# Kernel tuning notes

Hardware: AMD Instinct MI355X
Metric: run time of the kernel (lower is better)

The kernel has to match this reference:

```python
import jax, jax.numpy as jnp
import numpy as np

M, IN, OUT, K = 16384, 1024, 1024, 12


def setup_inputs() -> dict:
    key = jax.random.key(0)
    ks = jax.random.split(key, 7)
    x = jax.random.normal(ks[0], (M, IN), dtype=jnp.float32)
    # grid: per-feature linspace(-2,2) plus noise so the per-row sort is nontrivial
    base = jnp.linspace(-2.0, 2.0, K, dtype=jnp.float32)
    grid = jnp.broadcast_to(base, (IN, K)) + 0.3 * jax.random.normal(ks[1], (IN, K), dtype=jnp.float32)
    coeffs = 0.1 * jax.random.normal(ks[2], (IN, K), dtype=jnp.float32)
    knot_alive = 3.0 * jnp.ones((IN, K), dtype=jnp.float32) + 0.5 * jax.random.normal(ks[3], (IN, K), dtype=jnp.float32)
    proj_w = jax.random.normal(ks[4], (OUT, IN), dtype=jnp.float32) / np.sqrt(IN)
    proj_b = jax.random.normal(ks[5], (OUT,), dtype=jnp.float32) * 0.01
    res_w = jax.random.normal(ks[6], (OUT, IN), dtype=jnp.float32) / np.sqrt(IN)
    return {"x": x, "grid": grid, "coeffs": coeffs, "knot_alive": knot_alive,
            "proj_w": proj_w, "proj_b": proj_b, "res_w": res_w}


def _eval_adaptive_spline(x, grid, coeffs, knot_alive):
    # x: (M, in)  grid/coeffs/knot_alive: (in, K)
    K_ = grid.shape[1]
    sort_idx = jnp.argsort(grid, axis=1)
    sorted_grid = jnp.take_along_axis(grid, sort_idx, axis=1)
    sorted_coeffs = jnp.take_along_axis(coeffs, sort_idx, axis=1)
    sorted_alive = jnp.take_along_axis(knot_alive, sort_idx, axis=1)
    masked_coeffs = sorted_coeffs * jax.nn.sigmoid(sorted_alive)  # (in, K)

    grid_min = sorted_grid[:, 0]   # (in,)
    grid_max = sorted_grid[:, -1]  # (in,)
    x_clamped = jnp.minimum(jnp.maximum(x, grid_min[None, :]), grid_max[None, :])
    grid_range = jnp.maximum(grid_max - grid_min, 1e-6)
    x_norm = (x_clamped - grid_min[None, :]) / grid_range[None, :] * (K_ - 1)  # (M, in)
    idx_l = jnp.clip(x_norm.astype(jnp.int32), 0, K_ - 2)  # trunc == floor (x_norm >= 0)
    frac = x_norm - idx_l.astype(x.dtype)

    feat = jnp.arange(x.shape[1])[None, :]  # (1, in)
    c_left = masked_coeffs[feat, idx_l]      # (M, in)
    c_right = masked_coeffs[feat, idx_l + 1]  # (M, in)
    return c_left + frac * (c_right - c_left)


def reference(x, grid, coeffs, knot_alive, proj_w, proj_b, res_w):
    spline_out = _eval_adaptive_spline(x, grid, coeffs, knot_alive)  # (M, in)
    return spline_out @ proj_w.T + proj_b + x @ res_w.T  # (M, out)
```

## Files before the change

### kernel.cpp

```cpp
#include <hip/hip_runtime.h>
#include <hip/hip_bf16.h>

typedef unsigned short u16;
typedef float f32x4 __attribute__((ext_vector_type(4)));
typedef __bf16 bf16x8 __attribute__((ext_vector_type(8)));
typedef u16 u16x8 __attribute__((ext_vector_type(8)));

#define M_DIM 16384
#define IN_DIM 1024
#define OUT_DIM 1024
#define K_KNOTS 12
#define KCAT 2048


__device__ __forceinline__ u16 f2bf(float f) {
    unsigned int u = __builtin_bit_cast(unsigned int, f);
    u = u + 0x7FFFu + ((u >> 16) & 1u);
    return (u16)(u >> 16);
}

__device__ __forceinline__ void gload_lds16(const void* g, void* l) {
    __builtin_amdgcn_global_load_lds(
        (const __attribute__((address_space(1))) unsigned int*)g,
        (__attribute__((address_space(3))) unsigned int*)l, 16, 0, 0);
}

__global__ __launch_bounds__(256) void prep_conv_kernel(
    const float* __restrict__ grid,
    const float* __restrict__ coeffs,
    const float* __restrict__ alive,
    const float* __restrict__ pw,
    const float* __restrict__ rw,
    float* __restrict__ pmc,
    float* __restrict__ pgmin,
    float* __restrict__ pscale,
    u16* __restrict__ Bw)
{
    const int tid = threadIdx.x;
    if (blockIdx.x < 256) {
        const int n16 = blockIdx.x >> 2;
        const int jb  = (blockIdx.x & 3) * 4;
        #pragma unroll 1
        for (int j = jb; j < jb + 4; ++j) {
            int s = j * 256 + tid;
            int kc = s >> 6, l = s & 63;
            int row = n16 * 16 + (l & 15);
            int k = kc * 32 + ((l >> 4) & 3) * 8;
            const float* src = (k < IN_DIM) ? &pw[(long)row * IN_DIM + k]
                                            : &rw[(long)row * IN_DIM + (k - IN_DIM)];
            float4 v0 = *(const float4*)src;
            float4 v1 = *(const float4*)(src + 4);
            u16x8 ov;
            ov[0] = f2bf(v0.x); ov[1] = f2bf(v0.y); ov[2] = f2bf(v0.z); ov[3] = f2bf(v0.w);
            ov[4] = f2bf(v1.x); ov[5] = f2bf(v1.y); ov[6] = f2bf(v1.z); ov[7] = f2bf(v1.w);
            *(u16x8*)&Bw[((long)n16 * 64 + kc) * 512 + l * 8] = ov;
        }
    } else {
        int i = (blockIdx.x - 256) * 256 + tid;
        if (i >= IN_DIM) return;
        float g[K_KNOTS], c[K_KNOTS], a[K_KNOTS];
        for (int k = 0; k < K_KNOTS; ++k) {
            g[k] = grid[i * K_KNOTS + k];
            c[k] = coeffs[i * K_KNOTS + k];
            a[k] = alive[i * K_KNOTS + k];
        }
        for (int k = 1; k < K_KNOTS; ++k) {
            float gk = g[k], ck = c[k], ak = a[k];
            int j = k - 1;
            while (j >= 0 && g[j] > gk) {
                g[j + 1] = g[j]; c[j + 1] = c[j]; a[j + 1] = a[j]; --j;
            }
            g[j + 1] = gk; c[j + 1] = ck; a[j + 1] = ak;
        }
        for (int k = 0; k < K_KNOTS; ++k)
            pmc[i * K_KNOTS + k] = c[k] / (1.0f + expf(-a[k]));
        pgmin[i] = g[0];
        pscale[i] = (float)(K_KNOTS - 1) / fmaxf(g[K_KNOTS - 1] - g[0], 1e-6f);
    }
}

#define XT_STR 260

__global__ __launch_bounds__(512) void build_a_kernel(
    const float* __restrict__ x,
    const float* __restrict__ pmc,
    const float* __restrict__ pgmin,
    const float* __restrict__ pscale,
    u16* __restrict__ Abf)
{
    __shared__ float s_mc[256 * K_KNOTS];
    __shared__ float s_gmin[256];
    __shared__ float s_scale[256];
    __shared__ float xt[16 * XT_STR];
    const int tid = threadIdx.x;
    const int mp = blockIdx.x >> 2;
    const int c0 = (blockIdx.x & 3) * 256;

    for (int i = tid; i < 256 * K_KNOTS; i += 512) s_mc[i] = pmc[c0 * K_KNOTS + i];
    if (tid < 256) { s_gmin[tid] = pgmin[c0 + tid]; s_scale[tid] = pscale[c0 + tid]; }

    #pragma unroll 1
    for (int g = 0; g < 4; ++g) {
        const int m16 = mp * 4 + g;
        __syncthreads();

        #pragma unroll
        for (int p = 0; p < 2; ++p) {
            int idx = p * 512 + tid;
            int r = idx >> 6, lc = (idx & 63) * 4;
            *(float4*)&xt[r * XT_STR + lc] =
                *(const float4*)&x[(long)(m16 * 16 + r) * IN_DIM + c0 + lc];
        }
        __syncthreads();

        {
            int kc_l = tid >> 6, l = tid & 63;
            int r = l & 15;
            int cb = kc_l * 32 + ((l >> 4) & 3) * 8;
            const float* xp = &xt[r * XT_STR + cb];
            float4 v0 = *(const float4*)xp;
            float4 v1 = *(const float4*)(xp + 4);
            float xs[8] = {v0.x, v0.y, v0.z, v0.w, v1.x, v1.y, v1.z, v1.w};
            u16x8 so, co;
            #pragma unroll
            for (int e = 0; e < 8; ++e) {
                int il = cb + e;
                float xx = xs[e];
                float xn = (xx - s_gmin[il]) * s_scale[il];
                xn = fminf(fmaxf(xn, 0.0f), (float)(K_KNOTS - 1));
                int li = (int)xn;
                if (li > K_KNOTS - 2) li = K_KNOTS - 2;
                float frac = xn - (float)li;
                float cl = s_mc[il * K_KNOTS + li];
                float cr = s_mc[il * K_KNOTS + li + 1];
                so[e] = f2bf(cl + frac * (cr - cl));
                co[e] = f2bf(xx);
            }
            long kcS = (long)m16 * 64 + (c0 >> 5) + kc_l;
            *(u16x8*)&Abf[kcS * 512 + l * 8] = so;
            *(u16x8*)&Abf[(kcS + 32) * 512 + l * 8] = co;
        }
    }
}

#define TBK 32
#define NT (KCAT / TBK)
#define MSTR 32768L

#define BAR()     asm volatile("s_barrier" ::: "memory")
#define VM3BAR()  asm volatile("s_waitcnt vmcnt(3)\ns_barrier" ::: "memory")
#define LGKM0()   do { asm volatile("s_waitcnt lgkmcnt(0)" ::: "memory"); \
                       __builtin_amdgcn_sched_barrier(0); } while (0)

#define STAGE2(T, cb) do { \
    gload_lds16(pAf +          ((long)(T)) * 512, &lds[(cb) * 4096 + tid * 8]); \
    gload_lds16(pBf +          ((long)(T)) * 512, &lds[8192 + (cb) * 8192 + tid * 8]); \
    gload_lds16(pBf + 8*MSTR + ((long)(T)) * 512, &lds[8192 + (cb) * 8192 + 4096 + tid * 8]); } while (0)

__global__ __launch_bounds__(512, 4) void gemm_kernel(
    const u16* __restrict__ A,
    const u16* __restrict__ B,
    const float* __restrict__ bias,
    float* __restrict__ C)
{
    __shared__ __align__(16) u16 lds[24576];

    const int tid  = threadIdx.x;
    const int lane = tid & 63;
    const int wave = tid >> 6;
    const int wm   = wave >> 2;
    const int wn   = wave & 3;

    int wgid = (blockIdx.x & 7) * 64 + (blockIdx.x >> 3);
    const int brow = (wgid >> 2) * 128;
    const int bcol = (wgid & 3) * 256;

    const u16* pAf = A + ((long)(brow >> 4) + wave) * MSTR + lane * 8;
    const u16* pBf = B + ((long)(bcol >> 4) + wave) * MSTR + lane * 8;

    const int loff = lane * 8;

    f32x4 acc[4][4] = {};
    bf16x8 af[4], bfr[4];

    STAGE2(0, 0);
    STAGE2(1, 1);
    VM3BAR();

    #pragma unroll 1
    for (int t = 0; t < NT; ++t) {
        const int cb = t & 1;
        const int ab = cb * 4096;
        const int bb = 8192 + cb * 8192;

        #pragma unroll
        for (int m_ = 0; m_ < 4; ++m_)
            af[m_] = *(const bf16x8*)&lds[ab + (wm * 4 + m_) * 512 + loff];
        #pragma unroll
        for (int n_ = 0; n_ < 4; ++n_)
            bfr[n_] = *(const bf16x8*)&lds[bb + (wn * 4 + n_) * 512 + loff];
        LGKM0();
        __builtin_amdgcn_s_setprio(1);
        #pragma unroll
        for (int m_ = 0; m_ < 4; ++m_)
            #pragma unroll
            for (int n_ = 0; n_ < 4; ++n_)
                acc[m_][n_] = __builtin_amdgcn_mfma_f32_16x16x32_bf16(
                    af[m_], bfr[n_], acc[m_][n_], 0, 0, 0);
        __builtin_amdgcn_s_setprio(0);
        BAR();

        const int T2 = (t + 2) & 63;
        STAGE2(T2, cb);
        VM3BAR();
    }

    const int crow0 = brow + wm * 64 + (lane >> 4) * 4;
    const int ccol0 = bcol + wn * 64 + (lane & 15);
    float bv[4];
    #pragma unroll
    for (int n = 0; n < 4; ++n) bv[n] = bias[ccol0 + n * 16];
    #pragma unroll
    for (int m = 0; m < 4; ++m) {
        #pragma unroll
        for (int n = 0; n < 4; ++n) {
            #pragma unroll
            for (int j = 0; j < 4; ++j) {
                int row = crow0 + m * 16 + j;
                C[(long)row * OUT_DIM + ccol0 + n * 16] = acc[m][n][j] + bv[n];
            }
        }
    }
}

extern "C" void kernel_launch(void* const* d_in, const int* in_sizes, int n_in,
                              void* d_out, int out_size, void* d_ws, size_t ws_size,
                              hipStream_t stream) {
    const float* x      = (const float*)d_in[0];
    const float* grid   = (const float*)d_in[1];
    const float* coeffs = (const float*)d_in[2];
    const float* alive  = (const float*)d_in[3];
    const float* proj_w = (const float*)d_in[4];
    const float* proj_b = (const float*)d_in[5];
    const float* res_w  = (const float*)d_in[6];
    float* out = (float*)d_out;

    char* w = (char*)d_ws;
    size_t a_bytes = (size_t)M_DIM * KCAT * sizeof(u16);
    size_t b_bytes = (size_t)OUT_DIM * KCAT * sizeof(u16);
    u16* Abf   = (u16*)w;
    u16* Bw    = (u16*)(w + a_bytes);
    float* pmc = (float*)(w + a_bytes + b_bytes);
    float* pgmin  = pmc + IN_DIM * K_KNOTS;
    float* pscale = pgmin + IN_DIM;

    prep_conv_kernel<<<260, 256, 0, stream>>>(grid, coeffs, alive, proj_w, res_w,
                                              pmc, pgmin, pscale, Bw);
    build_a_kernel<<<(M_DIM / 64) * 4, 512, 0, stream>>>(x, pmc, pgmin, pscale, Abf);
    gemm_kernel<<<(M_DIM / 128) * (OUT_DIM / 256), 512, 0, stream>>>(Abf, Bw, proj_b, out);
}
```

Measured before the change: 95.21 us.

## Fuse spline A-operand construction into GEMM main loop, drop build_a kernel

Removes the separate kernel that wrote a bf16 concatenated [spline|x] A matrix to global memory. Each GEMM workgroup now reads fp32 x directly, evaluates the spline (with gmin, scale and coeff lookups from global/cache) and writes the bf16 A fragment into LDS, prefetching the next x tile into registers. This avoids a 64MB A write and reread plus one launch. In exchange, each x row is recomputed by the 4 column-tile workgroups and the spline ALU work plus uncoalesced coefficient gathers now sit in the GEMM pipeline.

```diff
diff --git a/kernel.cpp b/kernel.cpp
--- a/kernel.cpp
+++ b/kernel.cpp
@@ -79,86 +79,85 @@
     }
 }
 
-#define XT_STR 260
-
-__global__ __launch_bounds__(512) void build_a_kernel(
+#define TBK 32
+#define NT (KCAT / TBK)
+#define MSTR 32768L
+
+#define BAR()     asm volatile("s_barrier" ::: "memory")
+#define LGKM0()   do { asm volatile("s_waitcnt lgkmcnt(0)" ::: "memory"); \
+                       __builtin_amdgcn_sched_barrier(0); } while (0)
+
+__device__ __forceinline__ void compute_a_frag(
+    int T2, float4 v0, float4 v1,
+    const float* __restrict__ pmc, const float* __restrict__ pgmin,
+    const float* __restrict__ pscale, int coff, u16* ldsdst)
+{
+    float xs[8] = {v0.x, v0.y, v0.z, v0.w, v1.x, v1.y, v1.z, v1.w};
+    u16x8 ov;
+    int kk = T2 * 32 + coff;
+    if (T2 < 32) {
+        float4 g0 = *(const float4*)&pgmin[kk];
+        float4 g1 = *(const float4*)&pgmin[kk + 4];
+        float4 s0 = *(const float4*)&pscale[kk];
+        float4 s1 = *(const float4*)&pscale[kk + 4];
+        float gm[8] = {g0.x, g0.y, g0.z, g0.w, g1.x, g1.y, g1.z, g1.w};
+        float sc[8] = {s0.x, s0.y, s0.z, s0.w, s1.x, s1.y, s1.z, s1.w};
+        #pragma unroll
+        for (int e = 0; e < 8; ++e) {
+            float xx = xs[e];
+            float xn = (xx - gm[e]) * sc[e];
+            xn = fminf(fmaxf(xn, 0.0f), (float)(K_KNOTS - 1));
+            int li = (int)xn;
+            if (li > K_KNOTS - 2) li = K_KNOTS - 2;
+            float fr = xn - (float)li;
+            const float* pc = &pmc[(long)(kk + e) * K_KNOTS + li];
+            float cl = pc[0], cr = pc[1];
+            ov[e] = f2bf(cl + fr * (cr - cl));
+        }
+    } else {
+        #pragma unroll
+        for (int e = 0; e < 8; ++e) ov[e] = f2bf(xs[e]);
+    }
+    *(u16x8*)ldsdst = ov;
+}
+
+#define XCOL(T) ((((T) < 32) ? (T) * 32 : (T) * 32 - 1024) + coff)
+
+#define PHASE(cb, T2v, T3v, XP0, XP1, XN0, XN1) do { \
+    const int ab = (cb) * 4096; \
+    const int bb = 8192 + (cb) * 8192; \
+    _Pragma("unroll") \
+    for (int m_ = 0; m_ < 4; ++m_) \
+        af[m_] = *(const bf16x8*)&lds[ab + (wm * 4 + m_) * 512 + loff]; \
+    _Pragma("unroll") \
+    for (int n_ = 0; n_ < 4; ++n_) \
+        bfr[n_] = *(const bf16x8*)&lds[bb + (wn * 4 + n_) * 512 + loff]; \
+    LGKM0(); \
+    __builtin_amdgcn_s_setprio(1); \
+    _Pragma("unroll") \
+    for (int m_ = 0; m_ < 4; ++m_) \
+        _Pragma("unroll") \
+        for (int n_ = 0; n_ < 4; ++n_) \
+            acc[m_][n_] = __builtin_amdgcn_mfma_f32_16x16x32_bf16( \
+                af[m_], bfr[n_], acc[m_][n_], 0, 0, 0); \
+    __builtin_amdgcn_s_setprio(0); \
+    BAR(); \
+    compute_a_frag((T2v), XP0, XP1, pmc, pgmin, pscale, coff, \
+                   (u16*)&lds[ab + tid * 8]); \
+    __builtin_amdgcn_sched_barrier(0); \
+    gload_lds16(pBf +            ((long)(T2v)) * 512, &lds[bb + tid * 8]); \
+    gload_lds16(pBf + 8 * MSTR + ((long)(T2v)) * 512, &lds[bb + 4096 + tid * 8]); \
+    { int xc_ = XCOL(T3v); \
+      XN0 = *(const float4*)&xrow[xc_]; \
+      XN1 = *(const float4*)&xrow[xc_ + 4]; } \
+    asm volatile("s_waitcnt vmcnt(4) lgkmcnt(0)\ns_barrier" ::: "memory"); \
+} while (0)
+
+__global__ __launch_bounds__(512, 4) void gemm_kernel(
     const float* __restrict__ x,
     const float* __restrict__ pmc,
     const float* __restrict__ pgmin,
     const float* __restrict__ pscale,
-    u16* __restrict__ Abf)
-{
-    __shared__ float s_mc[256 * K_KNOTS];
-    __shared__ float s_gmin[256];
-    __shared__ float s_scale[256];
-    __shared__ float xt[16 * XT_STR];
-    const int tid = threadIdx.x;
-    const int mp = blockIdx.x >> 2;
-    const int c0 = (blockIdx.x & 3) * 256;
-
-    for (int i = tid; i < 256 * K_KNOTS; i += 512) s_mc[i] = pmc[c0 * K_KNOTS + i];
-    if (tid < 256) { s_gmin[tid] = pgmin[c0 + tid]; s_scale[tid] = pscale[c0 + tid]; }
-
-    #pragma unroll 1
-    for (int g = 0; g < 4; ++g) {
-        const int m16 = mp * 4 + g;
-        __syncthreads();
-
-        #pragma unroll
-        for (int p = 0; p < 2; ++p) {
-            int idx = p * 512 + tid;
-            int r = idx >> 6, lc = (idx & 63) * 4;
-            *(float4*)&xt[r * XT_STR + lc] =
-                *(const float4*)&x[(long)(m16 * 16 + r) * IN_DIM + c0 + lc];
-        }
-        __syncthreads();
-
-        {
-            int kc_l = tid >> 6, l = tid & 63;
-            int r = l & 15;
-            int cb = kc_l * 32 + ((l >> 4) & 3) * 8;
-            const float* xp = &xt[r * XT_STR + cb];
-            float4 v0 = *(const float4*)xp;
-            float4 v1 = *(const float4*)(xp + 4);
-            float xs[8] = {v0.x, v0.y, v0.z, v0.w, v1.x, v1.y, v1.z, v1.w};
-            u16x8 so, co;
-            #pragma unroll
-            for (int e = 0; e < 8; ++e) {
-                int il = cb + e;
-                float xx = xs[e];
-                float xn = (xx - s_gmin[il]) * s_scale[il];
-                xn = fminf(fmaxf(xn, 0.0f), (float)(K_KNOTS - 1));
-                int li = (int)xn;
-                if (li > K_KNOTS - 2) li = K_KNOTS - 2;
-                float frac = xn - (float)li;
-                float cl = s_mc[il * K_KNOTS + li];
-                float cr = s_mc[il * K_KNOTS + li + 1];
-                so[e] = f2bf(cl + frac * (cr - cl));
-                co[e] = f2bf(xx);
-            }
-            long kcS = (long)m16 * 64 + (c0 >> 5) + kc_l;
-            *(u16x8*)&Abf[kcS * 512 + l * 8] = so;
-            *(u16x8*)&Abf[(kcS + 32) * 512 + l * 8] = co;
-        }
-    }
-}
-
-#define TBK 32
-#define NT (KCAT / TBK)
-#define MSTR 32768L
-
-#define BAR()     asm volatile("s_barrier" ::: "memory")
-#define VM3BAR()  asm volatile("s_waitcnt vmcnt(3)\ns_barrier" ::: "memory")
-#define LGKM0()   do { asm volatile("s_waitcnt lgkmcnt(0)" ::: "memory"); \
-                       __builtin_amdgcn_sched_barrier(0); } while (0)
-
-#define STAGE2(T, cb) do { \
-    gload_lds16(pAf +          ((long)(T)) * 512, &lds[(cb) * 4096 + tid * 8]); \
-    gload_lds16(pBf +          ((long)(T)) * 512, &lds[8192 + (cb) * 8192 + tid * 8]); \
-    gload_lds16(pBf + 8*MSTR + ((long)(T)) * 512, &lds[8192 + (cb) * 8192 + 4096 + tid * 8]); } while (0)
-
-__global__ __launch_bounds__(512, 4) void gemm_kernel(
-    const u16* __restrict__ A,
     const u16* __restrict__ B,
     const float* __restrict__ bias,
     float* __restrict__ C)
@@ -175,44 +174,34 @@
     const int brow = (wgid >> 2) * 128;
     const int bcol = (wgid & 3) * 256;
 
-    const u16* pAf = A + ((long)(brow >> 4) + wave) * MSTR + lane * 8;
     const u16* pBf = B + ((long)(bcol >> 4) + wave) * MSTR + lane * 8;
+    const float* xrow = x + (long)(brow + wave * 16 + (lane & 15)) * IN_DIM;
+    const int coff = ((lane >> 4) & 3) * 8;
 
     const int loff = lane * 8;
 
     f32x4 acc[4][4] = {};
     bf16x8 af[4], bfr[4];
-
-    STAGE2(0, 0);
-    STAGE2(1, 1);
-    VM3BAR();
+    float4 xa0, xa1, xb0, xb1;
+
+    { int xc_ = XCOL(0); xa0 = *(const float4*)&xrow[xc_]; xa1 = *(const float4*)&xrow[xc_ + 4]; }
+    { int xc_ = XCOL(1); xb0 = *(const float4*)&xrow[xc_]; xb1 = *(const float4*)&xrow[xc_ + 4]; }
+    compute_a_frag(0, xa0, xa1, pmc, pgmin, pscale, coff, (u16*)&lds[tid * 8]);
+    compute_a_frag(1, xb0, xb1, pmc, pgmin, pscale, coff, (u16*)&lds[4096 + tid * 8]);
+    __builtin_amdgcn_sched_barrier(0);
+    gload_lds16(pBf,                  &lds[8192 + tid * 8]);
+    gload_lds16(pBf + 8 * MSTR,       &lds[8192 + 4096 + tid * 8]);
+    gload_lds16(pBf + 512,            &lds[16384 + tid * 8]);
+    gload_lds16(pBf + 8 * MSTR + 512, &lds[16384 + 4096 + tid * 8]);
+    { int xc_ = XCOL(2); xa0 = *(const float4*)&xrow[xc_]; xa1 = *(const float4*)&xrow[xc_ + 4]; }
+    asm volatile("s_waitcnt vmcnt(4) lgkmcnt(0)\ns_barrier" ::: "memory");
 
     #pragma unroll 1
-    for (int t = 0; t < NT; ++t) {
-        const int cb = t & 1;
-        const int ab = cb * 4096;
-        const int bb = 8192 + cb * 8192;
-
-        #pragma unroll
-        for (int m_ = 0; m_ < 4; ++m_)
-            af[m_] = *(const bf16x8*)&lds[ab + (wm * 4 + m_) * 512 + loff];
-        #pragma unroll
-        for (int n_ = 0; n_ < 4; ++n_)
-            bfr[n_] = *(const bf16x8*)&lds[bb + (wn * 4 + n_) * 512 + loff];
-        LGKM0();
-        __builtin_amdgcn_s_setprio(1);
-        #pragma unroll
-        for (int m_ = 0; m_ < 4; ++m_)
-            #pragma unroll
-            for (int n_ = 0; n_ < 4; ++n_)
-                acc[m_][n_] = __builtin_amdgcn_mfma_f32_16x16x32_bf16(
-                    af[m_], bfr[n_], acc[m_][n_], 0, 0, 0);
-        __builtin_amdgcn_s_setprio(0);
-        BAR();
-
-        const int T2 = (t + 2) & 63;
-        STAGE2(T2, cb);
-        VM3BAR();
+    for (int t = 0; t < NT; t += 2) {
+        const int T2a = (t + 2) & 63, T3a = (t + 3) & 63;
+        PHASE(0, T2a, T3a, xa0, xa1, xb0, xb1);
+        const int T2b = (t + 3) & 63, T3b = (t + 4) & 63;
+        PHASE(1, T2b, T3b, xb0, xb1, xa0, xa1);
     }
 
     const int crow0 = brow + wm * 64 + (lane >> 4) * 4;
@@ -246,16 +235,14 @@
     float* out = (float*)d_out;
 
     char* w = (char*)d_ws;
-    size_t a_bytes = (size_t)M_DIM * KCAT * sizeof(u16);
     size_t b_bytes = (size_t)OUT_DIM * KCAT * sizeof(u16);
-    u16* Abf   = (u16*)w;
-    u16* Bw    = (u16*)(w + a_bytes);
-    float* pmc = (float*)(w + a_bytes + b_bytes);
+    u16* Bw    = (u16*)w;
+    float* pmc = (float*)(w + b_bytes);
     float* pgmin  = pmc + IN_DIM * K_KNOTS;
     float* pscale = pgmin + IN_DIM;
 
     prep_conv_kernel<<<260, 256, 0, stream>>>(grid, coeffs, alive, proj_w, res_w,
                                               pmc, pgmin, pscale, Bw);
-    build_a_kernel<<<(M_DIM / 64) * 4, 512, 0, stream>>>(x, pmc, pgmin, pscale, Abf);
-    gemm_kernel<<<(M_DIM / 128) * (OUT_DIM / 256), 512, 0, stream>>>(Abf, Bw, proj_b, out);
-}
+    gemm_kernel<<<(M_DIM / 128) * (OUT_DIM / 256), 512, 0, stream>>>(
+        x, pmc, pgmin, pscale, Bw, proj_b, out);
+}
```

Result: slower. 142.5 us (+49.6%).

## Fuse weight conversion and spline prep into the A-building kernel

Applied to the files above, without the earlier changes.

Merges the prep kernel (weight bf16 conversion plus per-feature knot sort) with the A-matrix build kernel into a single launch. The weight-conversion blocks become a separate group of 64 blocks, and every A-building block redoes the knot sort for its 256 features directly into shared memory instead of reading precomputed tables from global memory. This removes one kernel launch and the dependency between prep and build. In exchange the sort and sigmoid work is repeated across all 1024 build blocks.

```diff
diff --git a/kernel.cpp b/kernel.cpp
--- a/kernel.cpp
+++ b/kernel.cpp
@@ -25,24 +25,29 @@
         (__attribute__((address_space(3))) unsigned int*)l, 16, 0, 0);
 }
 
-__global__ __launch_bounds__(256) void prep_conv_kernel(
+#define XT_STR 260
+
+__global__ __launch_bounds__(512) void pre_kernel(
     const float* __restrict__ grid,
     const float* __restrict__ coeffs,
     const float* __restrict__ alive,
     const float* __restrict__ pw,
     const float* __restrict__ rw,
-    float* __restrict__ pmc,
-    float* __restrict__ pgmin,
-    float* __restrict__ pscale,
-    u16* __restrict__ Bw)
+    const float* __restrict__ x,
+    u16* __restrict__ Bw,
+    u16* __restrict__ Abf)
 {
+    __shared__ float s_mc[256 * K_KNOTS];
+    __shared__ float s_gmin[256];
+    __shared__ float s_scale[256];
+    __shared__ float xt[16 * XT_STR];
     const int tid = threadIdx.x;
-    if (blockIdx.x < 256) {
-        const int n16 = blockIdx.x >> 2;
-        const int jb  = (blockIdx.x & 3) * 4;
+
+    if (blockIdx.x < 64) {
+        const int n16 = blockIdx.x;
         #pragma unroll 1
-        for (int j = jb; j < jb + 4; ++j) {
-            int s = j * 256 + tid;
+        for (int it = 0; it < 8; ++it) {
+            int s = it * 512 + tid;
             int kc = s >> 6, l = s & 63;
             int row = n16 * 16 + (l & 15);
             int k = kc * 32 + ((l >> 4) & 3) * 8;
@@ -55,15 +60,23 @@
             ov[4] = f2bf(v1.x); ov[5] = f2bf(v1.y); ov[6] = f2bf(v1.z); ov[7] = f2bf(v1.w);
             *(u16x8*)&Bw[((long)n16 * 64 + kc) * 512 + l * 8] = ov;
         }
-    } else {
-        int i = (blockIdx.x - 256) * 256 + tid;
-        if (i >= IN_DIM) return;
+        return;
+    }
+
+    const int bid = blockIdx.x - 64;
+    const int mp = bid >> 2;
+    const int c0 = (bid & 3) * 256;
+
+    if (tid < 256) {
+        const int f = c0 + tid;
         float g[K_KNOTS], c[K_KNOTS], a[K_KNOTS];
+        #pragma unroll
         for (int k = 0; k < K_KNOTS; ++k) {
-            g[k] = grid[i * K_KNOTS + k];
-            c[k] = coeffs[i * K_KNOTS + k];
-            a[k] = alive[i * K_KNOTS + k];
-        }
+            g[k] = grid[f * K_KNOTS + k];
+            c[k] = coeffs[f * K_KNOTS + k];
+            a[k] = alive[f * K_KNOTS + k];
+        }
+        #pragma unroll 1
         for (int k = 1; k < K_KNOTS; ++k) {
             float gk = g[k], ck = c[k], ak = a[k];
             int j = k - 1;
@@ -72,32 +85,12 @@
             }
             g[j + 1] = gk; c[j + 1] = ck; a[j + 1] = ak;
         }
+        #pragma unroll
         for (int k = 0; k < K_KNOTS; ++k)
-            pmc[i * K_KNOTS + k] = c[k] / (1.0f + expf(-a[k]));
-        pgmin[i] = g[0];
-        pscale[i] = (float)(K_KNOTS - 1) / fmaxf(g[K_KNOTS - 1] - g[0], 1e-6f);
-    }
-}
-
-#define XT_STR 260
-
-__global__ __launch_bounds__(512) void build_a_kernel(
-    const float* __restrict__ x,
-    const float* __restrict__ pmc,
-    const float* __restrict__ pgmin,
-    const float* __restrict__ pscale,
-    u16* __restrict__ Abf)
-{
-    __shared__ float s_mc[256 * K_KNOTS];
-    __shared__ float s_gmin[256];
-    __shared__ float s_scale[256];
-    __shared__ float xt[16 * XT_STR];
-    const int tid = threadIdx.x;
-    const int mp = blockIdx.x >> 2;
-    const int c0 = (blockIdx.x & 3) * 256;
-
-    for (int i = tid; i < 256 * K_KNOTS; i += 512) s_mc[i] = pmc[c0 * K_KNOTS + i];
-    if (tid < 256) { s_gmin[tid] = pgmin[c0 + tid]; s_scale[tid] = pscale[c0 + tid]; }
+            s_mc[tid * K_KNOTS + k] = c[k] / (1.0f + expf(-a[k]));
+        s_gmin[tid] = g[0];
+        s_scale[tid] = (float)(K_KNOTS - 1) / fmaxf(g[K_KNOTS - 1] - g[0], 1e-6f);
+    }
 
     #pragma unroll 1
     for (int g = 0; g < 4; ++g) {
@@ -247,15 +240,11 @@
 
     char* w = (char*)d_ws;
     size_t a_bytes = (size_t)M_DIM * KCAT * sizeof(u16);
-    size_t b_bytes = (size_t)OUT_DIM * KCAT * sizeof(u16);
-    u16* Abf   = (u16*)w;
-    u16* Bw    = (u16*)(w + a_bytes);
-    float* pmc = (float*)(w + a_bytes + b_bytes);
-    float* pgmin  = pmc + IN_DIM * K_KNOTS;
-    float* pscale = pgmin + IN_DIM;
-
-    prep_conv_kernel<<<260, 256, 0, stream>>>(grid, coeffs, alive, proj_w, res_w,
-                                              pmc, pgmin, pscale, Bw);
-    build_a_kernel<<<(M_DIM / 64) * 4, 512, 0, stream>>>(x, pmc, pgmin, pscale, Abf);
-    gemm_kernel<<<(M_DIM / 128) * (OUT_DIM / 256), 512, 0, stream>>>(Abf, Bw, proj_b, out);
-}
+    u16* Abf = (u16*)w;
+    u16* Bw  = (u16*)(w + a_bytes);
+
+    pre_kernel<<<64 + (M_DIM / 64) * 4, 512, 0, stream>>>(
+        grid, coeffs, alive, proj_w, res_w, x, Bw, Abf);
+    gemm_kernel<<<(M_DIM / 128) * (OUT_DIM / 256), 512, 0, stream>>>(
+        Abf, Bw, proj_b, out);
+}
```

Result: slower. 106.3 us (+11.6%).
